# Kernel tuning notes

Measured on AMD Instinct MI355X. Metric: run time of the kernel, lower is better.

## Reference

```python
import jax, jax.numpy as jnp
import numpy as np

RADIUS = 2
TEMP = 1.0
B, CIN, D, H, W = 1, 32, 64, 64, 64
PROJ, OUT = 64, 64
K = (2 * RADIUS + 1) ** 3  # 125 local offsets

_OFFSETS = np.array([(dz, dy, dx)
                     for dz in range(-RADIUS, RADIUS + 1)
                     for dy in range(-RADIUS, RADIUS + 1)
                     for dx in range(-RADIUS, RADIUS + 1)], dtype=np.int32)


def _conv3d(x, w, b, pad):
    y = jax.lax.conv_general_dilated(
        x, w, window_strides=(1, 1, 1), padding=[(pad, pad)] * 3,
        dimension_numbers=('NCDHW', 'OIDHW', 'NCDHW'))
    if b is not None:
        y = y + b[None, :, None, None, None]
    return y


def _l2norm(x):
    # torch F.normalize(dim=1): x / max(||x||_2, 1e-12)
    n = jnp.sqrt(jnp.sum(x * x, axis=1, keepdims=True))
    return x / jnp.maximum(n, 1e-12)


def _inorm(x, eps=1e-5):
    # InstanceNorm3d (affine=False): normalize over spatial dims per (B,C)
    mu = jnp.mean(x, axis=(2, 3, 4), keepdims=True)
    var = jnp.mean((x - mu) ** 2, axis=(2, 3, 4), keepdims=True)
    return (x - mu) * jax.lax.rsqrt(var + eps)


def _ntn(x):
    return jnp.nan_to_num(x, nan=0.0, posinf=0.0, neginf=0.0)


def setup_inputs() -> dict:
    key = jax.random.key(0)
    ks = jax.random.split(key, 8)
    s = 0.05
    return {
        'source_features': jax.random.normal(ks[0], (B, CIN, D, H, W), jnp.float32),
        'warped_target_features': jax.random.normal(ks[1], (B, CIN, D, H, W), jnp.float32),
        'w_src': jax.random.normal(ks[2], (PROJ, CIN, 1, 1, 1), jnp.float32) * s,
        'b_src': jnp.zeros((PROJ,), jnp.float32),
        'w_tgt': jax.random.normal(ks[3], (PROJ, CIN, 1, 1, 1), jnp.float32) * s,
        'b_tgt': jnp.zeros((PROJ,), jnp.float32),
        'w_enc1': jax.random.normal(ks[4], (OUT, K + 5, 3, 3, 3), jnp.float32) * s,
        'b_enc1': jnp.zeros((OUT,), jnp.float32),
        'w_enc2': jax.random.normal(ks[5], (OUT, OUT, 3, 3, 3), jnp.float32) * s,
        'b_enc2': jnp.zeros((OUT,), jnp.float32),
    }


def reference(source_features, warped_target_features, w_src, b_src, w_tgt, b_tgt,
              w_enc1, b_enc1, w_enc2, b_enc2):
    sp = _l2norm(_conv3d(source_features, w_src, b_src, 0))      # [B,P,D,H,W]
    tp = _l2norm(_conv3d(warped_target_features, w_tgt, b_tgt, 0))
    pt = jnp.pad(tp, ((0, 0), (0, 0), (RADIUS, RADIUS), (RADIUS, RADIUS), (RADIUS, RADIUS)),
                 mode='edge')  # replicate pad

    starts = jnp.asarray(_OFFSETS + RADIUS, jnp.int32)  # [K,3] slice starts

    def corr_one(st):
        sh = jax.lax.dynamic_slice(pt, (0, 0, st[0], st[1], st[2]), (B, PROJ, D, H, W))
        return jnp.sum(sp * sh, axis=1)  # [B,D,H,W]

    corr = jnp.transpose(jax.vmap(corr_one)(starts), (1, 0, 2, 3, 4))  # [B,K,D,H,W]
    scaled = corr / max(TEMP, 1e-6)

    top2 = jax.lax.top_k(jnp.moveaxis(scaled, 1, -1), 2)[0]  # [B,D,H,W,2]
    m = jnp.moveaxis(top2[..., 0:1], -1, 1)   # running max   [B,1,D,H,W]
    s2 = jnp.moveaxis(top2[..., 1:2], -1, 1)  # second max

    p = jnp.exp(scaled - m)                    # [B,K,D,H,W]
    Z = jnp.sum(p, axis=1, keepdims=True)
    inv = 1.0 / jnp.maximum(Z, 1e-8)

    offv = jnp.asarray(_OFFSETS, jnp.float32)  # [K,3]
    expected_offset = _ntn(jnp.einsum('bkdhw,kc->bcdhw', p, offv) * inv)
    confidence = _ntn(jnp.minimum(inv, 1.0))   # max-prob = exp(m-m)/Z
    second_prob = jnp.exp(s2 - m) * inv
    margin = _ntn(jnp.maximum(confidence - second_prob, 0.0))
    entropy = _ntn(m + jnp.log(jnp.maximum(Z, 1e-8))
                   - jnp.sum(p * scaled, axis=1, keepdims=True) * inv)

    enc_in = jnp.concatenate([corr, expected_offset, confidence, entropy], axis=1)  # [B,K+5,D,H,W]
    h = _conv3d(enc_in, w_enc1, b_enc1, 1)
    h = jax.nn.gelu(_inorm(h), approximate=False)
    h = _conv3d(h, w_enc2, b_enc2, 1)
    h = jax.nn.gelu(_inorm(h), approximate=False)
    encoded_features = _ntn(h)

    return expected_offset, confidence, margin, entropy, encoded_features
```

## Files before the change

kernel.cpp:

```cpp
#include <hip/hip_runtime.h>

#define DEV __device__ __forceinline__

typedef short bf16x8 __attribute__((ext_vector_type(8)));
typedef float f32x4 __attribute__((ext_vector_type(4)));

static const int NVOX = 262144;

DEV float bflo(unsigned int u) { return __uint_as_float(u << 16); }
DEV float bfhi(unsigned int u) { return __uint_as_float(u & 0xffff0000u); }
DEV float bf2f(unsigned short s) { return __uint_as_float(((unsigned int)s) << 16); }
DEV unsigned short f2bf(float f) {
    unsigned int x = __float_as_uint(f);
    x += 0x7fffu + ((x >> 16) & 1u);
    return (unsigned short)(x >> 16);
}
DEV float ldin(const void* p, int i, int f) {
    return f ? ((const float*)p)[i] : bf2f(((const unsigned short*)p)[i]);
}

DEV void gld16(const unsigned short* g, unsigned short* l) {
    __builtin_amdgcn_global_load_lds(
        (const __attribute__((address_space(1))) unsigned int*)g,
        (__attribute__((address_space(3))) unsigned int*)l, 16, 0, 0);
}

__global__ void sniff_kernel(const unsigned short* __restrict__ src, int* __restrict__ flag) {
    __shared__ int cnt[256];
    int t = threadIdx.x;
    int c = 0;
    for (int i = t; i < 4096; i += 256) {
        unsigned int u = (unsigned int)src[i] & 0x7fffu;
        c += (u >= 0x4900u) ? 1 : 0;
    }
    cnt[t] = c;
    __syncthreads();
    for (int s = 128; s > 0; s >>= 1) {
        if (t < s) cnt[t] += cnt[t + s];
        __syncthreads();
    }
    if (t == 0) *flag = (cnt[0] > 8) ? 1 : 0;
}

__global__ void prep_kernel(const void* __restrict__ w1, const void* __restrict__ w2,
                            const void* __restrict__ bsv, const void* __restrict__ btv,
                            const void* __restrict__ b1v, const void* __restrict__ b2v,
                            const int* __restrict__ flag,
                            unsigned short* __restrict__ Wf1,
                            unsigned short* __restrict__ Wf2,
                            float* __restrict__ fbias) {
    const int f = *flag;
    int idx = blockIdx.x * 256 + threadIdx.x;
    const int N1  = 27 * 4 * 4 * 512;
    const int N1E = 2 * 4 * 512;
    const int N2  = 27 * 2 * 4 * 512;
    if (idx < N1) {
        int frag = idx >> 9;
        int r    = idx & 511;
        int lane = r >> 3, j = r & 7;
        int nt = frag & 3;
        int tk = frag >> 2;
        int tap = tk >> 2, kc = tk & 3;
        int o  = nt * 16 + (lane & 15);
        int cp = kc * 32 + (lane >> 4) * 8 + j;
        Wf1[idx] = f2bf(ldin(w1, (o * 130 + cp) * 27 + tap, f));
    } else if (idx < N1 + N1E) {
        int i2 = idx - N1;
        int frag = i2 >> 9;
        int r    = i2 & 511;
        int lane = r >> 3, j = r & 7;
        int nt = frag & 3, kc = frag >> 2;
        int o   = nt * 16 + (lane & 15);
        int kap = kc * 32 + (lane >> 4) * 8 + j;
        unsigned short val = 0;
        if (kap < 54) {
            int tap = kap >> 1, ch = 128 + (kap & 1);
            val = f2bf(ldin(w1, (o * 130 + ch) * 27 + tap, f));
        }
        Wf1[idx] = val;
    } else if (idx < N1 + N1E + N2) {
        int i2 = idx - N1 - N1E;
        int frag = i2 >> 9;
        int r    = i2 & 511;
        int lane = r >> 3, j = r & 7;
        int nt = frag & 3;
        int tk = frag >> 2;
        int tap = tk >> 1, kc = tk & 1;
        int o = nt * 16 + (lane & 15);
        int c = kc * 32 + (lane >> 4) * 8 + j;
        Wf2[i2] = f2bf(ldin(w2, (o * 64 + c) * 27 + tap, f));
    } else if (idx < N1 + N1E + N2 + 256) {
        int j = idx - N1 - N1E - N2;
        const void* bp = (j < 64) ? bsv : (j < 128) ? btv : (j < 192) ? b1v : b2v;
        fbias[j] = ldin(bp, j & 63, f);
    }
}

__global__ __launch_bounds__(256) void proj_kernel(
        const void* __restrict__ Xsrc, const void* __restrict__ Xtgt,
        const void* __restrict__ Wsrc, const void* __restrict__ Wtgt,
        const float* __restrict__ fbias, const int* __restrict__ flag,
        unsigned short* __restrict__ SP, unsigned short* __restrict__ TP) {
    const int f = *flag;
    const void* Xin = blockIdx.y ? Xtgt : Xsrc;
    const void* W   = blockIdx.y ? Wtgt : Wsrc;
    const float* Bb = fbias + (blockIdx.y ? 64 : 0);
    unsigned short* Outp = blockIdx.y ? TP : SP;

    __shared__ float ws[2048];
    const int t = threadIdx.x;
    for (int i = t; i < 2048; i += 256) {
        int ci = i >> 6, o = i & 63;
        ws[i] = ldin(W, o * 32 + ci, f);
    }
    __syncthreads();

    const size_t v = (size_t)blockIdx.x * 256 + t;
    float acc[64];
#pragma unroll
    for (int o = 0; o < 64; ++o) acc[o] = Bb[o];
    if (f) {
        const float* Xf = (const float*)Xin;
        for (int ci = 0; ci < 32; ++ci) {
            float x = Xf[(size_t)ci * NVOX + v];
            const float4* wr = (const float4*)(ws + ci * 64);
#pragma unroll
            for (int o4 = 0; o4 < 16; ++o4) {
                float4 w4 = wr[o4];
                acc[o4 * 4 + 0] = fmaf(w4.x, x, acc[o4 * 4 + 0]);
                acc[o4 * 4 + 1] = fmaf(w4.y, x, acc[o4 * 4 + 1]);
                acc[o4 * 4 + 2] = fmaf(w4.z, x, acc[o4 * 4 + 2]);
                acc[o4 * 4 + 3] = fmaf(w4.w, x, acc[o4 * 4 + 3]);
            }
        }
    } else {
        const unsigned short* Xb = (const unsigned short*)Xin;
        for (int ci = 0; ci < 32; ++ci) {
            float x = bf2f(Xb[(size_t)ci * NVOX + v]);
            const float4* wr = (const float4*)(ws + ci * 64);
#pragma unroll
            for (int o4 = 0; o4 < 16; ++o4) {
                float4 w4 = wr[o4];
                acc[o4 * 4 + 0] = fmaf(w4.x, x, acc[o4 * 4 + 0]);
                acc[o4 * 4 + 1] = fmaf(w4.y, x, acc[o4 * 4 + 1]);
                acc[o4 * 4 + 2] = fmaf(w4.z, x, acc[o4 * 4 + 2]);
                acc[o4 * 4 + 3] = fmaf(w4.w, x, acc[o4 * 4 + 3]);
            }
        }
    }
    float s = 0.f;
#pragma unroll
    for (int o = 0; o < 64; ++o) s = fmaf(acc[o], acc[o], s);
    float scale = 1.f / fmaxf(sqrtf(s), 1e-12f);

    unsigned int pk[32];
#pragma unroll
    for (int o = 0; o < 32; ++o)
        pk[o] = (unsigned int)f2bf(acc[2 * o] * scale) |
                ((unsigned int)f2bf(acc[2 * o + 1] * scale) << 16);
    uint4* outp = (uint4*)(Outp + v * 64);
#pragma unroll
    for (int j = 0; j < 8; ++j)
        outp[j] = make_uint4(pk[4 * j], pk[4 * j + 1], pk[4 * j + 2], pk[4 * j + 3]);
}

__global__ __launch_bounds__(256) void corr_kernel(
        const unsigned short* __restrict__ SP, const unsigned short* __restrict__ TP,
        unsigned short* __restrict__ X1, float* __restrict__ Out) {
    __shared__ __align__(16) unsigned short tpb[2][80 * 64];
    __shared__ __align__(16) unsigned short stage[64 * 128];

    const int t = threadIdx.x;
    const int wv = t >> 6, lane = t & 63;
    const int q = lane >> 4, l16 = lane & 15;
    const int x0 = wv * 16;

    const int bid = blockIdx.x;
    const int wg = (bid & 7) * 512 + (bid >> 3);
    const int z = wg >> 6, y = wg & 63;
    const size_t vbase = ((size_t)z * 64 + y) * 64;

    const unsigned short* arow = SP + (vbase + x0 + l16) * 64 + q * 8;
    const bf16x8 a0 = *(const bf16x8*)(arow);
    const bf16x8 a1 = *(const bf16x8*)(arow + 32);

    auto stage_tp = [&](int it, int b) {
        const int zc = min(max(z + it / 5 - 2, 0), 63);
        const int yc = min(max(y + it % 5 - 2, 0), 63);
        const unsigned short* tb = TP + ((size_t)zc * 64 + yc) * 4096;
#pragma unroll
        for (int j = 0; j < 2; ++j) {
            int c = t + j * 256;
            int pp = c >> 3, cc = c & 7;
            int xc = min(max(pp - 2, 0), 63);
            gld16(tb + xc * 64 + ((cc ^ (pp & 7)) * 8),
                  &tpb[b][(wv * 64 + j * 256) * 8]);
        }
        if (wv < 2) {
            int c = 512 + wv * 64 + lane;
            int pp = c >> 3, cc = c & 7;
            int xc = min(max(pp - 2, 0), 63);
            gld16(tb + xc * 64 + ((cc ^ (pp & 7)) * 8),
                  &tpb[b][(512 + wv * 64) * 8]);
        }
    };

    stage_tp(0, 0);
    __syncthreads();

    int p = 0;
    for (int it = 0; it < 25; ++it) {
        if (it < 24) stage_tp(it + 1, p ^ 1);

        f32x4 acc[2] = {{0.f, 0.f, 0.f, 0.f}, {0.f, 0.f, 0.f, 0.f}};
        {
            const char* tb = (const char*)tpb[p];
#pragma unroll
            for (int nt = 0; nt < 2; ++nt) {
                const int pr = x0 + nt * 16 + l16;
                bf16x8 b0 = *(const bf16x8*)(tb + pr * 128 + ((q ^ (pr & 7)) * 16));
                bf16x8 b1 = *(const bf16x8*)(tb + pr * 128 + (((4 + q) ^ (pr & 7)) * 16));
                acc[nt] = __builtin_amdgcn_mfma_f32_16x16x32_bf16(a0, b0, acc[nt], 0, 0, 0);
                acc[nt] = __builtin_amdgcn_mfma_f32_16x16x32_bf16(a1, b1, acc[nt], 0, 0, 0);
            }
        }
        const int kb = it * 5;
        char* sg = (char*)stage;
#pragma unroll
        for (int nt = 0; nt < 2; ++nt) {
#pragma unroll
            for (int r = 0; r < 4; ++r) {
                int ml = q * 4 + r;
                int dxp = nt * 16 + l16 - ml;
                if ((unsigned)dxp < 5u) {
                    int xl = x0 + ml;
                    *(unsigned short*)(sg + xl * 256 + (((kb + dxp) * 2) ^ ((xl & 7) << 4))) =
                        f2bf(acc[nt][r]);
                }
            }
        }
        __syncthreads();
        p ^= 1;
    }

    {
        const int vox = t >> 2, part = t & 3;
        const int sx = (vox & 7) << 4;
        const char* sg = (const char*)stage;
        uint4 u[4];
#pragma unroll
        for (int j = 0; j < 4; ++j)
            u[j] = *(const uint4*)(sg + vox * 256 + ((part * 64 + j * 16) ^ sx));

        float m = -1e30f, s2 = -1e30f;
#pragma unroll
        for (int j = 0; j < 4; ++j) {
            const unsigned int uu[4] = {u[j].x, u[j].y, u[j].z, u[j].w};
#pragma unroll
            for (int w = 0; w < 4; ++w) {
                int k = part * 32 + j * 8 + w * 2;
                float d0 = (k < 125) ? bflo(uu[w]) : -1e30f;
                float d1 = (k + 1 < 125) ? bfhi(uu[w]) : -1e30f;
                float lo0 = fminf(d0, m); m = fmaxf(d0, m); s2 = fmaxf(s2, lo0);
                float lo1 = fminf(d1, m); m = fmaxf(d1, m); s2 = fmaxf(s2, lo1);
            }
        }
#pragma unroll
        for (int off = 1; off <= 2; off <<= 1) {
            float om = __shfl_xor(m, off, 64);
            float os = __shfl_xor(s2, off, 64);
            float lo = fminf(m, om);
            m = fmaxf(m, om);
            s2 = fmaxf(fmaxf(s2, os), lo);
        }
        int kk = part * 32;
        int dz0 = kk / 25, rem = kk - dz0 * 25, dy0 = rem / 5, dx0 = rem - dy0 * 5;
        float fx = (float)(dx0 - 2), fy = (float)(dy0 - 2), fz = (float)(dz0 - 2);
        float Zs = 0.f, S1 = 0.f, Ox = 0.f, Oy = 0.f, Oz = 0.f;
#pragma unroll
        for (int j = 0; j < 4; ++j) {
            const unsigned int uu[4] = {u[j].x, u[j].y, u[j].z, u[j].w};
#pragma unroll
            for (int w = 0; w < 8; ++w) {
                int k = part * 32 + j * 8 + w;
                bool ok = (k < 125);
                float d = (w & 1) ? bfhi(uu[w >> 1]) : bflo(uu[w >> 1]);
                d = ok ? d : 0.f;
                float e = ok ? __expf(d - m) : 0.f;
                Zs += e; S1 = fmaf(e, d, S1);
                Ox = fmaf(e, fx, Ox); Oy = fmaf(e, fy, Oy); Oz = fmaf(e, fz, Oz);
                fx += 1.f;
                if (fx > 2.5f) { fx = -2.f; fy += 1.f; if (fy > 2.5f) { fy = -2.f; fz += 1.f; } }
            }
        }
#pragma unroll
        for (int off = 1; off <= 2; off <<= 1) {
            Zs += __shfl_xor(Zs, off, 64);
            S1 += __shfl_xor(S1, off, 64);
            Ox += __shfl_xor(Ox, off, 64);
            Oy += __shfl_xor(Oy, off, 64);
            Oz += __shfl_xor(Oz, off, 64);
        }
        if (part == 0) {
            float inv  = 1.f / fmaxf(Zs, 1e-8f);
            float eoz = Oz * inv, eoy = Oy * inv, eox = Ox * inv;
            float conf = fminf(inv, 1.f);
            float marg = fmaxf(conf - __expf(s2 - m) * inv, 0.f);
            float ent  = m + __logf(fmaxf(Zs, 1e-8f)) - S1 * inv;
            char* sgw = (char*)stage;
            *(unsigned short*)(sgw + vox * 256 + (250 ^ sx)) = f2bf(eoz);
            *(unsigned short*)(sgw + vox * 256 + (252 ^ sx)) = f2bf(eoy);
            *(unsigned short*)(sgw + vox * 256 + (254 ^ sx)) = f2bf(eox);
            const size_t v = vbase + vox;
            *(unsigned int*)(X1 + v * 160 + 128) =
                (unsigned int)f2bf(conf) | ((unsigned int)f2bf(ent) << 16);
            Out[v]                    = eoz;
            Out[(size_t)NVOX + v]     = eoy;
            Out[(size_t)2 * NVOX + v] = eox;
            Out[(size_t)3 * NVOX + v] = conf;
            Out[(size_t)4 * NVOX + v] = marg;
            Out[(size_t)5 * NVOX + v] = ent;
        }
    }
    __syncthreads();

#pragma unroll
    for (int j = 0; j < 4; ++j) {
        int i = t + j * 256;
        int vox = i >> 4, cc = i & 15;
        *(uint4*)(X1 + (vbase + vox) * 160 + (size_t)cc * 8) =
            *(const uint4*)((const char*)stage + vox * 256 + ((cc * 16) ^ ((vox & 7) << 4)));
    }
}

template <int XSTRIDE, int CPAD, int KC, int NLD, int MINW, bool TAIL>
__global__ __launch_bounds__(256, MINW) void conv3_kernel(
        const unsigned short* __restrict__ Xin, const unsigned short* __restrict__ Wf,
        const unsigned short* __restrict__ Wfe,
        const float* __restrict__ Bias, unsigned short* __restrict__ Out) {
    __shared__ __align__(16) unsigned short rowbuf[2][66 * CPAD];
    const int lin = blockIdx.x;
    const int z = (lin & 7) * 8 + ((lin >> 3) >> 6);
    const int y = (lin >> 3) & 63;
    const int t = threadIdx.x;
    const int wv = t >> 6, lane = t & 63;
    const int quad = lane >> 4, l16 = lane & 15;
    const int mt2 = (wv & 1) * 2;
    const int nt2 = (wv >> 1) * 2;
    const int CH16 = CPAD / 8;

    f32x4 acc[2][2] = {{{0.f,0.f,0.f,0.f},{0.f,0.f,0.f,0.f}},
                       {{0.f,0.f,0.f,0.f},{0.f,0.f,0.f,0.f}}};

    auto stage_row = [&](int zz, int yy, int b) {
        const unsigned short* base = Xin + (((size_t)zz * 64 + yy) * 64) * XSTRIDE;
#pragma unroll
        for (int i = 0; i < NLD; ++i) {
            int chunk = wv * 64 + lane + i * 256;
            int xi = chunk / CH16 + 1;
            int cc = chunk % CH16;
            gld16(base + (xi - 1) * XSTRIDE + ((cc ^ (xi & 7)) * 8),
                  &rowbuf[b][CPAD + (size_t)(wv * 64 + i * 256) * 8]);
        }
    };

    {
        const int zz = z - 1, yy = y - 1;
        if ((unsigned)zz < 64u && (unsigned)yy < 64u) stage_row(zz, yy, 0);
    }

    if (TAIL) {
        unsigned short* ebuf = &rowbuf[1][0];
#pragma unroll
        for (int i2 = 0; i2 < 8; ++i2) {
            int i = t + i2 * 256;
            int vox = i >> 5, slot = i & 31;
            unsigned int val = 0u;
            int kap;
            if (slot < 27) {
                int dz = slot / 9 - 1, dy = (slot / 3) % 3 - 1, dxx = slot % 3 - 1;
                int zz = z + dz, yy = y + dy, xx = vox + dxx;
                kap = slot * 2;
                if ((unsigned)zz < 64u && (unsigned)yy < 64u && (unsigned)xx < 64u)
                    val = *(const unsigned int*)(Xin + (((size_t)zz * 64 + yy) * 64 + xx) * XSTRIDE + 128);
            } else {
                kap = 54 + (slot - 27) * 2;
            }
            *(unsigned int*)(ebuf + vox * 72 + kap) = val;
        }
        __syncthreads();
#pragma unroll
        for (int kc = 0; kc < 2; ++kc) {
            bf16x8 bte[2];
#pragma unroll
            for (int nl = 0; nl < 2; ++nl)
                bte[nl] = *(const bf16x8*)(Wfe + (size_t)(kc * 4 + nt2 + nl) * 512 + lane * 8);
#pragma unroll
            for (int ml = 0; ml < 2; ++ml) {
                bf16x8 a = *(const bf16x8*)(ebuf + ((mt2 + ml) * 16 + l16) * 72 + (kc * 4 + quad) * 8);
#pragma unroll
                for (int nl = 0; nl < 2; ++nl)
                    acc[ml][nl] = __builtin_amdgcn_mfma_f32_16x16x32_bf16(a, bte[nl], acc[ml][nl], 0, 0, 0);
            }
        }
        __syncthreads();
    }

    if (t < 4 * CH16) {
        int b = t / (2 * CH16), r2 = (t / CH16) & 1, c = t % CH16;
        *(uint4*)(&rowbuf[b][(size_t)(r2 * 65) * CPAD + c * 8]) = make_uint4(0u, 0u, 0u, 0u);
    }
    __syncthreads();

    int p = 0;
    for (int it = 0; it < 9; ++it) {
        if (it < 8) {
            const int z2 = z + (it + 1) / 3 - 1, y2 = y + (it + 1) % 3 - 1;
            if ((unsigned)z2 < 64u && (unsigned)y2 < 64u) stage_row(z2, y2, p ^ 1);
        }
        const int zz = z + it / 3 - 1, yy = y + it % 3 - 1;
        if ((unsigned)zz < 64u && (unsigned)yy < 64u) {
            const unsigned short* rp = rowbuf[p];
#pragma unroll
            for (int dx = 0; dx < 3; ++dx) {
                const int tap = it * 3 + dx;
                const unsigned short* wt = Wf + ((size_t)tap * KC * 4) * 512 + lane * 8;
                bf16x8 bf[KC][2];
#pragma unroll
                for (int kc = 0; kc < KC; ++kc)
#pragma unroll
                    for (int nl = 0; nl < 2; ++nl)
                        bf[kc][nl] = *(const bf16x8*)(wt + (size_t)(kc * 4 + nt2 + nl) * 512);
#pragma unroll
                for (int kc = 0; kc < KC; ++kc) {
#pragma unroll
                    for (int ml = 0; ml < 2; ++ml) {
                        const int row = (mt2 + ml) * 16 + l16 + dx;
                        bf16x8 a = *(const bf16x8*)(&rp[(size_t)row * CPAD + ((kc * 4 + quad) ^ (row & 7)) * 8]);
#pragma unroll
                        for (int nl = 0; nl < 2; ++nl)
                            acc[ml][nl] = __builtin_amdgcn_mfma_f32_16x16x32_bf16(a, bf[kc][nl], acc[ml][nl], 0, 0, 0);
                    }
                }
            }
        }
        __syncthreads();
        p ^= 1;
    }

    const size_t vbase = ((size_t)z * 64 + y) * 64;
#pragma unroll
    for (int ml = 0; ml < 2; ++ml) {
#pragma unroll
        for (int nl = 0; nl < 2; ++nl) {
            const int oc = (nt2 + nl) * 16 + l16;
            const float bv = Bias[oc];
#pragma unroll
            for (int r = 0; r < 4; ++r)
                Out[(vbase + (mt2 + ml) * 16 + quad * 4 + r) * 64 + oc] = f2bf(acc[ml][nl][r] + bv);
        }
    }
}

__global__ __launch_bounds__(256) void stats_kernel(
        const unsigned short* __restrict__ H, float* __restrict__ stats) {
    const int t = threadIdx.x;
    const int c = t & 63, g = t >> 6;
    float s = 0.f, q = 0.f;
    for (int v = blockIdx.x * 4 + g; v < NVOX; v += gridDim.x * 4) {
        float x = bf2f(H[(size_t)v * 64 + c]);
        s += x; q = fmaf(x, x, q);
    }
    __shared__ float ls[256], lq[256];
    ls[t] = s; lq[t] = q;
    __syncthreads();
    if (t < 64) {
        s = ls[t] + ls[t + 64] + ls[t + 128] + ls[t + 192];
        q = lq[t] + lq[t + 64] + lq[t + 128] + lq[t + 192];
        atomicAdd(&stats[c], s);
        atomicAdd(&stats[64 + c], q);
    }
}

__global__ void finalize_kernel(const float* __restrict__ stats, float* __restrict__ musr) {
    int c = threadIdx.x;
    if (c < 64) {
        float mu  = stats[c] * (1.0f / 262144.0f);
        float var = stats[64 + c] * (1.0f / 262144.0f) - mu * mu;
        musr[c] = mu;
        musr[64 + c] = rsqrtf(var + 1e-5f);
    }
}

__global__ __launch_bounds__(256) void norm_gelu_kernel(
        const unsigned short* __restrict__ H, const float* __restrict__ musr,
        unsigned short* __restrict__ G) {
    const size_t base = ((size_t)blockIdx.x * 256 + threadIdx.x) * 8;
    uint4 u = *(const uint4*)(H + base);
    const int c0 = (int)(base & 63);
    const unsigned int uu[4] = {u.x, u.y, u.z, u.w};
    unsigned int w[4];
#pragma unroll
    for (int p = 0; p < 4; ++p) {
        int c = c0 + p * 2;
        float x0 = (bflo(uu[p]) - musr[c]) * musr[64 + c];
        float x1 = (bfhi(uu[p]) - musr[c + 1]) * musr[64 + c + 1];
        float g0 = 0.5f * x0 * (1.f + erff(x0 * 0.70710678118f));
        float g1 = 0.5f * x1 * (1.f + erff(x1 * 0.70710678118f));
        w[p] = (unsigned int)f2bf(g0) | ((unsigned int)f2bf(g1) << 16);
    }
    *(uint4*)(G + base) = make_uint4(w[0], w[1], w[2], w[3]);
}

__global__ __launch_bounds__(256) void out_final_kernel(
        const unsigned short* __restrict__ H2, const float* __restrict__ musr,
        float* __restrict__ OutEnc) {
    __shared__ float tile[64 * 260];
    const int t = threadIdx.x;
    const size_t v0 = (size_t)blockIdx.x * 256;
#pragma unroll
    for (int i = 0; i < 8; ++i) {
        int chunk = t + i * 256;
        uint4 u = *(const uint4*)(H2 + v0 * 64 + (size_t)chunk * 8);
        int vox = chunk >> 3;
        int c0 = (chunk & 7) * 8;
        const unsigned int uu[4] = {u.x, u.y, u.z, u.w};
#pragma unroll
        for (int p = 0; p < 4; ++p) {
            int c = c0 + p * 2;
            float x0 = (bflo(uu[p]) - musr[c]) * musr[64 + c];
            float x1 = (bfhi(uu[p]) - musr[c + 1]) * musr[64 + c + 1];
            tile[c * 260 + vox]       = 0.5f * x0 * (1.f + erff(x0 * 0.70710678118f));
            tile[(c + 1) * 260 + vox] = 0.5f * x1 * (1.f + erff(x1 * 0.70710678118f));
        }
    }
    __syncthreads();
    const int c = t >> 2, sub = t & 3;
#pragma unroll
    for (int iter = 0; iter < 16; ++iter) {
        int fq = iter * 4 + sub;
        float4 val = *(const float4*)(&tile[c * 260 + fq * 4]);
        *(float4*)(OutEnc + (size_t)c * NVOX + v0 + fq * 4) = val;
    }
}

extern "C" void kernel_launch(void* const* d_in, const int* in_sizes, int n_in,
                              void* d_out, int out_size, void* d_ws, size_t ws_size,
                              hipStream_t stream) {
    const void* src  = d_in[0];
    const void* tgt  = d_in[1];
    const void* wsrc = d_in[2];
    const void* bsrc = d_in[3];
    const void* wtgt = d_in[4];
    const void* btgt = d_in[5];
    const void* w1   = d_in[6];
    const void* b1   = d_in[7];
    const void* w2   = d_in[8];
    const void* b2   = d_in[9];
    float* out = (float*)d_out;

    char* ws = (char*)d_ws;
    unsigned short* TPb = (unsigned short*)(ws);
    unsigned short* SPb = (unsigned short*)(ws + 33554432);
    unsigned short* X1  = (unsigned short*)(ws + 67108864);
    unsigned short* Wf1 = (unsigned short*)(ws + 150994944);
    unsigned short* Wf2 = (unsigned short*)(ws + 151547904);
    int*   flag   = (int*)  (ws + 151769088);
    float* fbias  = (float*)(ws + 151769152);
    float* stats1 = (float*)(ws + 151770176);
    float* musr1  = (float*)(ws + 151770688);
    float* stats2 = (float*)(ws + 151771200);
    float* musr2  = (float*)(ws + 151771712);
    unsigned short* H1 = SPb;
    unsigned short* G1 = TPb;
    unsigned short* H2 = X1;
    unsigned short* Wf1e = Wf1 + 27 * 4 * 4 * 512;

    (void)hipMemsetAsync(stats1, 0, 2048, stream);
    sniff_kernel<<<1, 256, 0, stream>>>((const unsigned short*)src, flag);
    prep_kernel<<<1313, 256, 0, stream>>>(w1, w2, bsrc, btgt, b1, b2, flag, Wf1, Wf2, fbias);
    proj_kernel<<<dim3(1024, 2), 256, 0, stream>>>(src, tgt, wsrc, wtgt, fbias, flag, SPb, TPb);
    corr_kernel<<<4096, 256, 0, stream>>>(SPb, TPb, X1, out);
    conv3_kernel<160, 128, 4, 4, 4, true><<<4096, 256, 0, stream>>>(X1, Wf1, Wf1e, fbias + 128, H1);
    stats_kernel<<<256, 256, 0, stream>>>(H1, stats1);
    finalize_kernel<<<1, 64, 0, stream>>>(stats1, musr1);
    norm_gelu_kernel<<<8192, 256, 0, stream>>>(H1, musr1, G1);
    conv3_kernel<64, 64, 2, 2, 6, false><<<4096, 256, 0, stream>>>(G1, Wf2, nullptr, fbias + 192, H2);
    stats_kernel<<<256, 256, 0, stream>>>(H2, stats2);
    finalize_kernel<<<1, 64, 0, stream>>>(stats2, musr2);
    out_final_kernel<<<1024, 256, 0, stream>>>(H2, musr2, out + 6 * (size_t)NVOX);
}
```

Baseline: 758.0 us.

## Compute two output rows per conv block, sharing weights and staged input planes

Each conv3 block now produces two adjacent y rows instead of one. It stages input rows into a 3-slot LDS ring so each staged plane serves both output rows, and it reuses every loaded weight fragment for twice as many MFMAs. The grid halves and launch-bound occupancy hints drop to match the higher register and LDS use. This cuts redundant input staging and weight loads but raises accumulator pressure and lowers occupancy.

Result: faster. 707.2 us (-6.7%).

```diff
diff --git a/kernel.cpp b/kernel.cpp
--- a/kernel.cpp
+++ b/kernel.cpp
@@ -338,55 +338,55 @@
         const unsigned short* __restrict__ Xin, const unsigned short* __restrict__ Wf,
         const unsigned short* __restrict__ Wfe,
         const float* __restrict__ Bias, unsigned short* __restrict__ Out) {
-    __shared__ __align__(16) unsigned short rowbuf[2][66 * CPAD];
+    constexpr int SLOT = 66 * CPAD;
+    constexpr int CH16 = CPAD / 8;
+    __shared__ __align__(16) unsigned short lds[3 * SLOT];
     const int lin = blockIdx.x;
-    const int z = (lin & 7) * 8 + ((lin >> 3) >> 6);
-    const int y = (lin >> 3) & 63;
+    const int wg = (lin & 7) * 256 + (lin >> 3);
+    const int z = wg >> 5;
+    const int y = (wg & 31) * 2;
     const int t = threadIdx.x;
     const int wv = t >> 6, lane = t & 63;
     const int quad = lane >> 4, l16 = lane & 15;
-    const int mt2 = (wv & 1) * 2;
+    const int ml2 = (wv & 1) * 2;
     const int nt2 = (wv >> 1) * 2;
-    const int CH16 = CPAD / 8;
-
-    f32x4 acc[2][2] = {{{0.f,0.f,0.f,0.f},{0.f,0.f,0.f,0.f}},
-                       {{0.f,0.f,0.f,0.f},{0.f,0.f,0.f,0.f}}};
-
-    auto stage_row = [&](int zz, int yy, int b) {
-        const unsigned short* base = Xin + (((size_t)zz * 64 + yy) * 64) * XSTRIDE;
+
+    f32x4 acc[2][2][2] = {};
+
+    auto stage_plane = [&](int pidx) {
+        const int zz = z + (pidx >> 2) - 1;
+        const int py = y + (pidx & 3) - 1;
+        if ((unsigned)zz >= 64u || (unsigned)py >= 64u) return;
+        const unsigned short* base = Xin + (((size_t)zz * 64 + py) * 64) * XSTRIDE;
+        unsigned short* dst = lds + (pidx % 3) * SLOT + CPAD;
 #pragma unroll
         for (int i = 0; i < NLD; ++i) {
             int chunk = wv * 64 + lane + i * 256;
-            int xi = chunk / CH16 + 1;
+            int xi = chunk / CH16;
             int cc = chunk % CH16;
-            gld16(base + (xi - 1) * XSTRIDE + ((cc ^ (xi & 7)) * 8),
-                  &rowbuf[b][CPAD + (size_t)(wv * 64 + i * 256) * 8]);
+            gld16(base + xi * XSTRIDE + ((cc ^ ((xi + 1) & 7)) * 8),
+                  dst + (size_t)(wv * 64 + i * 256) * 8);
         }
     };
 
-    {
-        const int zz = z - 1, yy = y - 1;
-        if ((unsigned)zz < 64u && (unsigned)yy < 64u) stage_row(zz, yy, 0);
-    }
-
     if (TAIL) {
-        unsigned short* ebuf = &rowbuf[1][0];
-#pragma unroll
-        for (int i2 = 0; i2 < 8; ++i2) {
+        unsigned short* ebuf = lds;
+#pragma unroll
+        for (int i2 = 0; i2 < 16; ++i2) {
             int i = t + i2 * 256;
             int vox = i >> 5, slot = i & 31;
             unsigned int val = 0u;
             int kap;
             if (slot < 27) {
-                int dz = slot / 9 - 1, dy = (slot / 3) % 3 - 1, dxx = slot % 3 - 1;
-                int zz = z + dz, yy = y + dy, xx = vox + dxx;
+                int ddz = slot / 9 - 1, ddy = (slot / 3) % 3 - 1, dxx = slot % 3 - 1;
+                int zz = z + ddz, yy = y + (vox >> 6) + ddy, xx = (vox & 63) + dxx;
                 kap = slot * 2;
                 if ((unsigned)zz < 64u && (unsigned)yy < 64u && (unsigned)xx < 64u)
                     val = *(const unsigned int*)(Xin + (((size_t)zz * 64 + yy) * 64 + xx) * XSTRIDE + 128);
             } else {
                 kap = 54 + (slot - 27) * 2;
             }
-            *(unsigned int*)(ebuf + vox * 72 + kap) = val;
+            *(unsigned int*)(ebuf + (size_t)vox * 72 + kap) = val;
         }
         __syncthreads();
 #pragma unroll
@@ -396,34 +396,48 @@
             for (int nl = 0; nl < 2; ++nl)
                 bte[nl] = *(const bf16x8*)(Wfe + (size_t)(kc * 4 + nt2 + nl) * 512 + lane * 8);
 #pragma unroll
+            for (int r = 0; r < 2; ++r)
+#pragma unroll
             for (int ml = 0; ml < 2; ++ml) {
-                bf16x8 a = *(const bf16x8*)(ebuf + ((mt2 + ml) * 16 + l16) * 72 + (kc * 4 + quad) * 8);
+                bf16x8 a = *(const bf16x8*)(ebuf + (size_t)(r * 64 + (ml2 + ml) * 16 + l16) * 72 + (kc * 4 + quad) * 8);
 #pragma unroll
                 for (int nl = 0; nl < 2; ++nl)
-                    acc[ml][nl] = __builtin_amdgcn_mfma_f32_16x16x32_bf16(a, bte[nl], acc[ml][nl], 0, 0, 0);
+                    acc[r][ml][nl] = __builtin_amdgcn_mfma_f32_16x16x32_bf16(a, bte[nl], acc[r][ml][nl], 0, 0, 0);
             }
         }
         __syncthreads();
     }
 
-    if (t < 4 * CH16) {
-        int b = t / (2 * CH16), r2 = (t / CH16) & 1, c = t % CH16;
-        *(uint4*)(&rowbuf[b][(size_t)(r2 * 65) * CPAD + c * 8]) = make_uint4(0u, 0u, 0u, 0u);
-    }
+    if (t < 6 * CH16) {
+        int sl = t / (2 * CH16), r2 = (t / CH16) & 1, c = t % CH16;
+        *(uint4*)(&lds[(size_t)sl * SLOT + (size_t)(r2 * 65) * CPAD + c * 8]) =
+            make_uint4(0u, 0u, 0u, 0u);
+    }
+    stage_plane(0);
+    stage_plane(1);
     __syncthreads();
 
-    int p = 0;
-    for (int it = 0; it < 9; ++it) {
-        if (it < 8) {
-            const int z2 = z + (it + 1) / 3 - 1, y2 = y + (it + 1) % 3 - 1;
-            if ((unsigned)z2 < 64u && (unsigned)y2 < 64u) stage_row(z2, y2, p ^ 1);
-        }
-        const int zz = z + it / 3 - 1, yy = y + it % 3 - 1;
-        if ((unsigned)zz < 64u && (unsigned)yy < 64u) {
-            const unsigned short* rp = rowbuf[p];
+    for (int i = 0; i < 9; ++i) {
+        const int s0 = (i / 3) * 4 + i % 3;
+        if (i == 3 || i == 6) {
+            stage_plane(s0 + 1);
+            stage_plane(s0 + 2);
+            __syncthreads();
+        } else if (s0 + 2 < 12) {
+            stage_plane(s0 + 2);
+        }
+
+        const int zz = z + i / 3 - 1;
+        const int dy = i % 3 - 1;
+        const bool zok = (unsigned)zz < 64u;
+        const bool rok0 = zok && (unsigned)(y + dy) < 64u;
+        const bool rok1 = zok && (unsigned)(y + 1 + dy) < 64u;
+        const unsigned short* sb0 = lds + (size_t)(s0 % 3) * SLOT;
+        const unsigned short* sb1 = lds + (size_t)((s0 + 1) % 3) * SLOT;
+        if (rok0 || rok1) {
 #pragma unroll
             for (int dx = 0; dx < 3; ++dx) {
-                const int tap = it * 3 + dx;
+                const int tap = (i / 3) * 9 + (i % 3) * 3 + dx;
                 const unsigned short* wt = Wf + ((size_t)tap * KC * 4) * 512 + lane * 8;
                 bf16x8 bf[KC][2];
 #pragma unroll
@@ -435,29 +449,41 @@
                 for (int kc = 0; kc < KC; ++kc) {
 #pragma unroll
                     for (int ml = 0; ml < 2; ++ml) {
-                        const int row = (mt2 + ml) * 16 + l16 + dx;
-                        bf16x8 a = *(const bf16x8*)(&rp[(size_t)row * CPAD + ((kc * 4 + quad) ^ (row & 7)) * 8]);
-#pragma unroll
-                        for (int nl = 0; nl < 2; ++nl)
-                            acc[ml][nl] = __builtin_amdgcn_mfma_f32_16x16x32_bf16(a, bf[kc][nl], acc[ml][nl], 0, 0, 0);
+                        const int row = (ml2 + ml) * 16 + l16 + dx;
+                        const int co = ((kc * 4 + quad) ^ (row & 7)) * 8;
+                        if (rok0) {
+                            bf16x8 a = *(const bf16x8*)(&sb0[(size_t)row * CPAD + co]);
+#pragma unroll
+                            for (int nl = 0; nl < 2; ++nl)
+                                acc[0][ml][nl] = __builtin_amdgcn_mfma_f32_16x16x32_bf16(a, bf[kc][nl], acc[0][ml][nl], 0, 0, 0);
+                        }
+                        if (rok1) {
+                            bf16x8 a = *(const bf16x8*)(&sb1[(size_t)row * CPAD + co]);
+#pragma unroll
+                            for (int nl = 0; nl < 2; ++nl)
+                                acc[1][ml][nl] = __builtin_amdgcn_mfma_f32_16x16x32_bf16(a, bf[kc][nl], acc[1][ml][nl], 0, 0, 0);
+                        }
                     }
                 }
             }
         }
         __syncthreads();
-        p ^= 1;
-    }
-
-    const size_t vbase = ((size_t)z * 64 + y) * 64;
-#pragma unroll
-    for (int ml = 0; ml < 2; ++ml) {
-#pragma unroll
-        for (int nl = 0; nl < 2; ++nl) {
-            const int oc = (nt2 + nl) * 16 + l16;
-            const float bv = Bias[oc];
-#pragma unroll
-            for (int r = 0; r < 4; ++r)
-                Out[(vbase + (mt2 + ml) * 16 + quad * 4 + r) * 64 + oc] = f2bf(acc[ml][nl][r] + bv);
+    }
+
+#pragma unroll
+    for (int r = 0; r < 2; ++r) {
+        const size_t vb = ((size_t)z * 64 + (y + r)) * 64;
+#pragma unroll
+        for (int ml = 0; ml < 2; ++ml) {
+#pragma unroll
+            for (int nl = 0; nl < 2; ++nl) {
+                const int oc = (nt2 + nl) * 16 + l16;
+                const float bv = Bias[oc];
+#pragma unroll
+                for (int rr = 0; rr < 4; ++rr)
+                    Out[(vb + (ml2 + ml) * 16 + quad * 4 + rr) * 64 + oc] =
+                        f2bf(acc[r][ml][nl][rr] + bv);
+            }
         }
     }
 }
@@ -581,11 +607,11 @@
     prep_kernel<<<1313, 256, 0, stream>>>(w1, w2, bsrc, btgt, b1, b2, flag, Wf1, Wf2, fbias);
     proj_kernel<<<dim3(1024, 2), 256, 0, stream>>>(src, tgt, wsrc, wtgt, fbias, flag, SPb, TPb);
     corr_kernel<<<4096, 256, 0, stream>>>(SPb, TPb, X1, out);
-    conv3_kernel<160, 128, 4, 4, 4, true><<<4096, 256, 0, stream>>>(X1, Wf1, Wf1e, fbias + 128, H1);
+    conv3_kernel<160, 128, 4, 4, 3, true><<<2048, 256, 0, stream>>>(X1, Wf1, Wf1e, fbias + 128, H1);
     stats_kernel<<<256, 256, 0, stream>>>(H1, stats1);
     finalize_kernel<<<1, 64, 0, stream>>>(stats1, musr1);
     norm_gelu_kernel<<<8192, 256, 0, stream>>>(H1, musr1, G1);
-    conv3_kernel<64, 64, 2, 2, 6, false><<<4096, 256, 0, stream>>>(G1, Wf2, nullptr, fbias + 192, H2);
+    conv3_kernel<64, 64, 2, 2, 4, false><<<2048, 256, 0, stream>>>(G1, Wf2, nullptr, fbias + 192, H2);
     stats_kernel<<<256, 256, 0, stream>>>(H2, stats2);
     finalize_kernel<<<1, 64, 0, stream>>>(stats2, musr2);
     out_final_kernel<<<1024, 256, 0, stream>>>(H2, musr2, out + 6 * (size_t)NVOX);
```
